# Performance work log

Hardware: AMD Instinct MI355X
Metric: run time of the kernel (lower is better)

Reference implementation:

```python
import jax, jax.numpy as jnp
import numpy as np

B, L, LTXT = 4, 1024, 128
D_MODEL, TEXT_DIM = 768, 768
D_INNER, D_STATE, D_CONV, DT_RANK = 2 * D_MODEL, 16, 4, (D_MODEL + 15) // 16


def setup_inputs() -> dict:
    key = jax.random.key(0)
    ks = jax.random.split(key, 10)
    s = 0.02
    f32 = jnp.float32
    # A_log init as in mamba_ssm: A = repeat(arange(1, d_state+1))
    A_log = jnp.log(jnp.broadcast_to(jnp.arange(1, D_STATE + 1, dtype=f32), (D_INNER, D_STATE)))
    return {
        "image_tokens": jax.random.normal(ks[0], (B, L, D_MODEL), f32),
        "text_tokens": jax.random.normal(ks[1], (B, LTXT, TEXT_DIM), f32),
        "W_txt": s * jax.random.normal(ks[2], (D_MODEL, TEXT_DIM), f32),
        "b_txt": jnp.zeros((D_MODEL,), f32),
        "in_proj_w": s * jax.random.normal(ks[3], (2 * D_INNER, D_MODEL), f32),
        "conv_w": s * jax.random.normal(ks[4], (D_INNER, 1, D_CONV), f32),
        "conv_b": jnp.zeros((D_INNER,), f32),
        "x_proj_w": s * jax.random.normal(ks[5], (DT_RANK + 2 * D_STATE, D_INNER), f32),
        "dt_proj_w": s * jax.random.normal(ks[6], (D_INNER, DT_RANK), f32),
        "dt_proj_b": jnp.full((D_INNER,), -4.6, f32),  # inv-softplus of small dt init
        "A_log": A_log,
        "D": jnp.ones((D_INNER,), f32),
        "out_proj_w": s * jax.random.normal(ks[7], (D_MODEL, D_INNER), f32),
    }


def _mamba(tokens, in_proj_w, conv_w, conv_b, x_proj_w, dt_proj_w, dt_proj_b, A_log, D, out_proj_w):
    Bsz = tokens.shape[0]
    # input projection -> x, z each (B, L, d_inner)
    xz = tokens @ in_proj_w.T
    x, z = jnp.split(xz, 2, axis=-1)
    # causal depthwise conv1d over L + SiLU
    x_bdl = jnp.transpose(x, (0, 2, 1))  # (B, d_inner, L)
    x_conv = jax.lax.conv_general_dilated(
        x_bdl, conv_w, (1,), [(D_CONV - 1, 0)],
        dimension_numbers=("NCH", "OIH", "NCH"), feature_group_count=D_INNER,
    ) + conv_b[None, :, None]
    x = jax.nn.silu(jnp.transpose(x_conv, (0, 2, 1)))  # (B, L, d_inner)
    # input-dependent SSM params
    x_dbl = x @ x_proj_w.T  # (B, L, dt_rank + 2*d_state)
    dt_r = x_dbl[..., :DT_RANK]
    Bm = x_dbl[..., DT_RANK:DT_RANK + D_STATE]  # (B, L, d_state)
    Cm = x_dbl[..., DT_RANK + D_STATE:]         # (B, L, d_state)
    dt = jax.nn.softplus(dt_r @ dt_proj_w.T + dt_proj_b)  # (B, L, d_inner)
    A = -jnp.exp(A_log)  # (d_inner, d_state)

    def step(h, inp):
        dt_t, B_t, C_t, u_t = inp  # (B,d_inner),(B,d_state),(B,d_state),(B,d_inner)
        dA = jnp.exp(dt_t[:, :, None] * A)                  # (B, d_inner, d_state)
        h = dA * h + (dt_t * u_t)[:, :, None] * B_t[:, None, :]
        y = jnp.einsum("bds,bs->bd", h, C_t)
        return h, y

    h0 = jnp.zeros((Bsz, D_INNER, D_STATE), tokens.dtype)
    xs = (
        jnp.transpose(dt, (1, 0, 2)),
        jnp.transpose(Bm, (1, 0, 2)),
        jnp.transpose(Cm, (1, 0, 2)),
        jnp.transpose(x, (1, 0, 2)),
    )
    _, ys = jax.lax.scan(step, h0, xs)  # ys: (L, B, d_inner)
    y = jnp.transpose(ys, (1, 0, 2)) + x * D
    y = y * jax.nn.silu(z)
    return y @ out_proj_w.T  # (B, L, d_model)


def reference(image_tokens, text_tokens, W_txt, b_txt, in_proj_w, conv_w, conv_b,
              x_proj_w, dt_proj_w, dt_proj_b, A_log, D, out_proj_w):
    # text_pool='cls' -> take token 0
    txt = text_tokens[:, 0, :] @ W_txt.T + b_txt          # (B, d_model)
    tokens = image_tokens + txt[:, None, :]                # broadcast add
    y = _mamba(tokens, in_proj_w, conv_w, conv_b, x_proj_w,
               dt_proj_w, dt_proj_b, A_log, D, out_proj_w)
    # AdaptiveAvgPool1d(1) over sequence dim, then squeeze -> (B, d_model)
    return y.mean(axis=1)
```

## Files before the change

### kernel.cpp

```cpp
#include <hip/hip_runtime.h>
#include <math.h>

constexpr int kB   = 4;
constexpr int kL   = 1024;
constexpr int kDM  = 768;
constexpr int kDI  = 1536;
constexpr int kDS  = 16;
constexpr int kDTR = 48;
constexpr int kNX  = 80;
constexpr int kM   = kB * kL;
constexpr int kLTXT = 128;

typedef __attribute__((ext_vector_type(8))) short bf16x8;
typedef __attribute__((ext_vector_type(4))) float f32x4;
typedef __attribute__((ext_vector_type(8))) unsigned short u16x8;

__device__ inline unsigned short f2bf(float f) {
    unsigned u = __float_as_uint(f);
    u = (u + 0x7FFFu + ((u >> 16) & 1u)) >> 16;
    return (unsigned short)u;
}
__device__ inline float bf2f(unsigned short us) {
    return __uint_as_float((unsigned)us << 16);
}

__device__ __forceinline__ void gl2lds16(const unsigned short* g, unsigned short* l) {
    __builtin_amdgcn_global_load_lds(
        (const __attribute__((address_space(1))) unsigned int*)g,
        (__attribute__((address_space(3))) unsigned int*)l, 16, 0, 0);
}

__global__ __launch_bounds__(256) void txt_kernel(
    const float* __restrict__ text, const float* __restrict__ Wt,
    const float* __restrict__ bt, float* __restrict__ txt)
{
    int gw = blockIdx.x * 4 + (threadIdx.x >> 6);
    int lane = threadIdx.x & 63;
    int b = gw / kDM;
    int j = gw - b * kDM;
    const float* trow = text + (size_t)b * kLTXT * kDM;
    const float* wrow = Wt + (size_t)j * kDM;
    float acc = 0.f;
    for (int k = lane; k < kDM; k += 64) acc = fmaf(trow[k], wrow[k], acc);
    #pragma unroll
    for (int o = 32; o; o >>= 1) acc += __shfl_xor(acc, o, 64);
    if (lane == 0) txt[gw] = acc + bt[j];
}

__global__ __launch_bounds__(256) void prep_kernel(
    const float* __restrict__ img, const float* __restrict__ txt,
    unsigned short* __restrict__ tok,
    const float* __restrict__ w, unsigned short* __restrict__ wb)
{
    const int bid = blockIdx.x;
    if (bid < 3072) {
        int i = bid * 256 + threadIdx.x;
        float4 a = ((const float4*)img)[i];
        int m = i / (kDM / 4);
        int k4 = i - m * (kDM / 4);
        float4 tv = ((const float4*)(txt + (size_t)(m >> 10) * kDM))[k4];
        ushort4 o;
        o.x = f2bf(a.x + tv.x); o.y = f2bf(a.y + tv.y);
        o.z = f2bf(a.z + tv.z); o.w = f2bf(a.w + tv.w);
        ((ushort4*)tok)[i] = o;
    } else {
        int i = (bid - 3072) * 256 + threadIdx.x;
        float4 a = ((const float4*)w)[i];
        ushort4 v;
        v.x = f2bf(a.x); v.y = f2bf(a.y); v.z = f2bf(a.z); v.w = f2bf(a.w);
        ((ushort4*)wb)[i] = v;
    }
}

__global__ __launch_bounds__(256) void mfma_inproj_kernel(
    const unsigned short* __restrict__ A, const unsigned short* __restrict__ W,
    float* __restrict__ xout, unsigned short* __restrict__ gout)
{
    __shared__ unsigned short Asm[2][128][32];
    __shared__ unsigned short Wsm[2][128][32];
    const int t = threadIdx.x;
    const int lane = t & 63;
    const int wv = t >> 6;
    const int wr = wv >> 1, wc = wv & 1;
    const int m0 = blockIdx.x * 128;
    const int n0 = blockIdx.y * 128;

    const int srow = lane >> 2;
    const int scol = (lane & 3) * 8;
    const unsigned short* agp  = A + (size_t)(m0 + wv * 32 + srow) * kDM + scol;
    const unsigned short* agp2 = agp + 16 * kDM;
    const unsigned short* wgp  = W + (size_t)(n0 + wv * 32 + srow) * kDM + scol;
    const unsigned short* wgp2 = wgp + 16 * kDM;

    auto stage = [&](int buf, int k0) {
        gl2lds16(agp  + k0, &Asm[buf][wv * 32][0]);
        gl2lds16(agp2 + k0, &Asm[buf][wv * 32 + 16][0]);
        gl2lds16(wgp  + k0, &Wsm[buf][wv * 32][0]);
        gl2lds16(wgp2 + k0, &Wsm[buf][wv * 32 + 16][0]);
    };

    f32x4 acc[4][4] = {};
    const int fr = lane & 15;
    const int fk = (lane >> 4) * 8;

    stage(0, 0);
    __syncthreads();

    int buf = 0;
    for (int k0 = 0; k0 < kDM; k0 += 32) {
        if (k0 + 32 < kDM) stage(buf ^ 1, k0 + 32);
        bf16x8 af[4], wf[4];
        #pragma unroll
        for (int i = 0; i < 4; ++i)
            af[i] = *(const bf16x8*)&Asm[buf][wr * 64 + i * 16 + fr][fk];
        #pragma unroll
        for (int j = 0; j < 4; ++j)
            wf[j] = *(const bf16x8*)&Wsm[buf][wc * 64 + j * 16 + fr][fk];
        #pragma unroll
        for (int i = 0; i < 4; ++i)
            #pragma unroll
            for (int j = 0; j < 4; ++j)
                acc[i][j] = __builtin_amdgcn_mfma_f32_16x16x32_bf16(af[i], wf[j], acc[i][j], 0, 0, 0);
        __syncthreads();
        buf ^= 1;
    }

    const int erow = (lane >> 4) * 4;
    const int ecol = lane & 15;
    #pragma unroll
    for (int i = 0; i < 4; ++i) {
        #pragma unroll
        for (int j = 0; j < 4; ++j) {
            const int gn = n0 + wc * 64 + j * 16 + ecol;
            #pragma unroll
            for (int q = 0; q < 4; ++q) {
                const int gm = m0 + wr * 64 + i * 16 + erow + q;
                float v = acc[i][j][q];
                if (gn < kDI) {
                    xout[(size_t)gm * kDI + gn] = v;
                } else {
                    gout[(size_t)gm * kDI + (gn - kDI)] = f2bf(v / (1.f + __expf(-v)));
                }
            }
        }
    }
}

constexpr int kKS   = 8;
constexpr int kKSEG = kDI / kKS;

__global__ __launch_bounds__(256) void xproj_splitk_kernel(
    const float* __restrict__ A, const float* __restrict__ W,
    float* __restrict__ part)
{
    __shared__ float As[16][68];
    __shared__ float Ws[16][84];
    const int t = threadIdx.x;
    const int m0 = blockIdx.x * 64;
    const int kbase = blockIdx.y * kKSEG;
    const int lrow = t >> 2, lk4 = (t & 3) << 2;
    const int ci = (t & 15) << 2;
    const int cj = (t >> 4) * 5;
    float acc[4][5] = {};
    const float* aptr = A + (size_t)(m0 + lrow) * kDI + kbase + lk4;

    for (int k0 = 0; k0 < kKSEG; k0 += 16) {
        float4 av = *(const float4*)(aptr + k0);
        if (k0) __syncthreads();
        As[lk4+0][lrow] = av.x; As[lk4+1][lrow] = av.y;
        As[lk4+2][lrow] = av.z; As[lk4+3][lrow] = av.w;
        #pragma unroll
        for (int i = 0; i < 5; ++i) {
            int idx = t + 256 * i;
            int n = idx % 80;
            int k = idx / 80;
            Ws[k][n] = W[(size_t)n * kDI + kbase + k0 + k];
        }
        __syncthreads();
        #pragma unroll
        for (int k = 0; k < 16; ++k) {
            const float4 a4 = *(const float4*)&As[k][ci];
            const float aa[4] = {a4.x, a4.y, a4.z, a4.w};
            float ww[5];
            #pragma unroll
            for (int j = 0; j < 5; ++j) ww[j] = Ws[k][cj + j];
            #pragma unroll
            for (int i = 0; i < 4; ++i)
                #pragma unroll
                for (int j = 0; j < 5; ++j)
                    acc[i][j] = fmaf(aa[i], ww[j], acc[i][j]);
        }
    }

    float* pbase = part + ((size_t)blockIdx.y * kM) * kNX;
    #pragma unroll
    for (int i = 0; i < 4; ++i)
        #pragma unroll
        for (int j = 0; j < 5; ++j)
            pbase[(size_t)(m0 + ci + i) * kNX + cj + j] = acc[i][j];
}

__global__ __launch_bounds__(256) void xproj_reduce_kernel(
    const float* __restrict__ part, float* __restrict__ xdbl)
{
    int i = blockIdx.x * 256 + threadIdx.x;
    float s = 0.f;
    #pragma unroll
    for (int k = 0; k < kKS; ++k) s += part[(size_t)k * kM * kNX + i];
    xdbl[i] = s;
}

__global__ __launch_bounds__(256) void dtproj_gemm_kernel(
    const float* __restrict__ A, const float* __restrict__ W,
    const float* __restrict__ bias, unsigned short* __restrict__ dt)
{
    __shared__ float As[16][68];
    __shared__ float Ws[16][68];
    const int t = threadIdx.x;
    const int m0 = blockIdx.x * 64;
    const int n0 = blockIdx.y * 64;
    const int lrow = t >> 2;
    const int lk4  = (t & 3) << 2;
    const int ci   = (t & 15) << 2;
    const int cj   = (t >> 4) << 2;
    float acc[4][4] = {};
    const float* aptr = A + (size_t)(m0 + lrow) * kNX + lk4;
    const float* wptr = W + (size_t)(n0 + lrow) * kDTR + lk4;

    for (int k0 = 0; k0 < kDTR; k0 += 16) {
        float4 av = *(const float4*)(aptr + k0);
        float4 wv = *(const float4*)(wptr + k0);
        if (k0) __syncthreads();
        As[lk4+0][lrow] = av.x; As[lk4+1][lrow] = av.y;
        As[lk4+2][lrow] = av.z; As[lk4+3][lrow] = av.w;
        Ws[lk4+0][lrow] = wv.x; Ws[lk4+1][lrow] = wv.y;
        Ws[lk4+2][lrow] = wv.z; Ws[lk4+3][lrow] = wv.w;
        __syncthreads();
        #pragma unroll
        for (int k = 0; k < 16; ++k) {
            const float4 a4 = *(const float4*)&As[k][ci];
            const float4 w4 = *(const float4*)&Ws[k][cj];
            const float aa[4] = {a4.x, a4.y, a4.z, a4.w};
            const float ww[4] = {w4.x, w4.y, w4.z, w4.w};
            #pragma unroll
            for (int i = 0; i < 4; ++i)
                #pragma unroll
                for (int j = 0; j < 4; ++j)
                    acc[i][j] = fmaf(aa[i], ww[j], acc[i][j]);
        }
    }

    #pragma unroll
    for (int i = 0; i < 4; ++i) {
        const int gm = m0 + ci + i;
        ushort4 o;
        unsigned short* op = (unsigned short*)&o;
        #pragma unroll
        for (int j = 0; j < 4; ++j) {
            float v = acc[i][j] + bias[n0 + cj + j];
            v = (v > 20.f) ? v : log1pf(__expf(v));
            op[j] = f2bf(v);
        }
        *(ushort4*)&dt[(size_t)gm * kDI + n0 + cj] = o;
    }
}

__global__ __launch_bounds__(256) void conv_silu_kernel(
    const float* __restrict__ xraw, const float* __restrict__ cw,
    const float* __restrict__ cb, float* __restrict__ xout)
{
    int i = blockIdx.x * 256 + threadIdx.x;
    int d4 = i % (kDI / 4);
    int ml = i / (kDI / 4);
    int l = ml & (kL - 1);
    const int d = d4 * 4;
    float4 acc = *(const float4*)&cb[d];
    const float* base = xraw + (size_t)ml * kDI + d - 3 * (size_t)kDI;
    float4 w0 = *(const float4*)&cw[(d + 0) * 4];
    float4 w1 = *(const float4*)&cw[(d + 1) * 4];
    float4 w2 = *(const float4*)&cw[(d + 2) * 4];
    float4 w3 = *(const float4*)&cw[(d + 3) * 4];
    const float wj[4][4] = {{w0.x, w1.x, w2.x, w3.x}, {w0.y, w1.y, w2.y, w3.y},
                            {w0.z, w1.z, w2.z, w3.z}, {w0.w, w1.w, w2.w, w3.w}};
    #pragma unroll
    for (int j = 0; j < 4; ++j) {
        if (l - 3 + j >= 0) {
            float4 xv = *(const float4*)(base + (size_t)j * kDI);
            acc.x = fmaf(xv.x, wj[j][0], acc.x);
            acc.y = fmaf(xv.y, wj[j][1], acc.y);
            acc.z = fmaf(xv.z, wj[j][2], acc.z);
            acc.w = fmaf(xv.w, wj[j][3], acc.w);
        }
    }
    acc.x /= (1.f + __expf(-acc.x));
    acc.y /= (1.f + __expf(-acc.y));
    acc.z /= (1.f + __expf(-acc.z));
    acc.w /= (1.f + __expf(-acc.w));
    *(float4*)&xout[(size_t)ml * kDI + d] = acc;
}

constexpr int kNSEG = 16;
constexpr int kSEGL = kL / kNSEG;
constexpr int kCT   = 16;
constexpr int kBD   = kB * kDI;
constexpr int kP    = kBD * 16;
constexpr float kLOG2E = 1.44269504089f;

__global__ __launch_bounds__(256, 6) void scan11_kernel(
    const float* __restrict__ u, const unsigned short* __restrict__ g,
    const unsigned short* __restrict__ dt, const float* __restrict__ xdbl,
    const float* __restrict__ A_log,
    float* __restrict__ PA, float* __restrict__ QA,
    float* __restrict__ accA, float* __restrict__ wcA,
    float* __restrict__ ugA)
{
    __shared__ float uS [kCT][64];
    __shared__ float gS [kCT][64];
    __shared__ float dtS[kCT][64];
    __shared__ float bcS[kCT][34];
    const int t = threadIdx.x;
    const int blk = blockIdx.x;
    const int seg = blk & (kNSEG - 1);
    const int bd  = blk >> 4;
    const int b   = bd / 24;
    const int d0  = (bd % 24) * 64;
    const int c   = t & 63;
    const int sq  = t >> 6;
    const int d   = d0 + c;
    const int lb  = seg * kSEGL;

    f32x4 Av;
    {
        float4 al = *(const float4*)&A_log[d * kDS + sq * 4];
        Av.x = -__expf(al.x) * kLOG2E;
        Av.y = -__expf(al.y) * kLOG2E;
        Av.z = -__expf(al.z) * kLOG2E;
        Av.w = -__expf(al.w) * kLOG2E;
    }

    const float* u_base           = u  + ((size_t)b << 10) * kDI + d0;
    const unsigned short* g_base  = g  + ((size_t)b << 10) * kDI + d0;
    const unsigned short* dt_base = dt + ((size_t)b << 10) * kDI + d0;
    const float* bc_base = xdbl + ((size_t)b << 10) * kNX + kDTR;
    const int sr = t >> 4, scn = (t & 15) * 4;
    const int hr = (t & 127) >> 3, hc = ((t & 127) & 7) * 8;
    const int rb = (t & 127) >> 3, cbo = ((t & 127) & 7) * 4;

    float4 ru, rbc;
    u16x8 rgd;
    auto load_chunk = [&](int l0) {
        ru = *(const float4*)(u_base + (size_t)(l0 + sr) * kDI + scn);
        if (t < 128) {
            rgd = *(const u16x8*)(g_base + (size_t)(l0 + hr) * kDI + hc);
            rbc = *(const float4*)(bc_base + (size_t)(l0 + rb) * kNX + cbo);
        } else {
            rgd = *(const u16x8*)(dt_base + (size_t)(l0 + hr) * kDI + hc);
        }
    };
    auto store_chunk = [&]() {
        *(float4*)&uS[sr][scn] = ru;
        float* dst = (t < 128) ? &gS[hr][hc] : &dtS[hr][hc];
        float4 lo, hi;
        lo.x = bf2f(rgd[0]); lo.y = bf2f(rgd[1]);
        lo.z = bf2f(rgd[2]); lo.w = bf2f(rgd[3]);
        hi.x = bf2f(rgd[4]); hi.y = bf2f(rgd[5]);
        hi.z = bf2f(rgd[6]); hi.w = bf2f(rgd[7]);
        *(float4*)(dst)     = lo;
        *(float4*)(dst + 4) = hi;
        if (t < 128) *(float4*)&bcS[rb][cbo] = rbc;
    };

    f32x4 h   = {0.f, 0.f, 0.f, 0.f};
    f32x4 cp  = {1.f, 1.f, 1.f, 1.f};
    f32x4 acc = {0.f, 0.f, 0.f, 0.f};
    f32x4 wc  = {0.f, 0.f, 0.f, 0.f};
    float ug = 0.f;

    load_chunk(lb);
    store_chunk();
    __syncthreads();

    #pragma unroll
    for (int ck = 0; ck < kSEGL / kCT; ++ck) {
        if (ck + 1 < kSEGL / kCT) load_chunk(lb + (ck + 1) * kCT);
        #pragma unroll 8
        for (int i = 0; i < kCT; ++i) {
            const float dtv = dtS[i][c];
            const float uv  = uS [i][c];
            const float gv  = gS [i][c];
            const f32x4 Bv = *(const f32x4*)&bcS[i][sq * 4];
            const f32x4 Cv = *(const f32x4*)&bcS[i][16 + sq * 4];
            const f32x4 pm = dtv * Av;
            f32x4 dA;
            dA.x = exp2f(pm.x); dA.y = exp2f(pm.y);
            dA.z = exp2f(pm.z); dA.w = exp2f(pm.w);
            const float dtu = dtv * uv;
            h  = dA * h + dtu * Bv;
            cp = cp * dA;
            const f32x4 cg = Cv * gv;
            acc = h * cg + acc;
            wc  = cp * cg + wc;
            ug  = fmaf(uv, gv, ug);
        }
        if (ck + 1 < kSEGL / kCT) {
            __syncthreads();
            store_chunk();
            __syncthreads();
        }
    }

    const size_t o = (size_t)seg * kP + ((size_t)sq * kBD + b * kDI + d) * 4;
    *(f32x4*)&PA[o]   = cp;
    *(f32x4*)&QA[o]   = h;
    *(f32x4*)&accA[o] = acc;
    *(f32x4*)&wcA[o]  = wc;
    if (sq == 0) ugA[(size_t)seg * kBD + b * kDI + d] = ug;
}

__global__ __launch_bounds__(256) void scan_combine_kernel(
    const float* __restrict__ PA, const float* __restrict__ QA,
    const float* __restrict__ accA, const float* __restrict__ wcA,
    const float* __restrict__ ugA, const float* __restrict__ Dvec,
    float* __restrict__ ysum)
{
    const int p = blockIdx.x * 256 + threadIdx.x;
    const int s = p & 15;
    const int bd = p >> 4;
    const size_t pbase = ((size_t)(s >> 2) * kBD + bd) * 4 + (s & 3);
    float h = 0.f, tot = 0.f;
    #pragma unroll
    for (int seg = 0; seg < kNSEG; ++seg) {
        const size_t o = (size_t)seg * kP + pbase;
        tot += accA[o] + h * wcA[o];
        h = fmaf(PA[o], h, QA[o]);
    }
    #pragma unroll
    for (int o2 = 1; o2 < 16; o2 <<= 1) tot += __shfl_xor(tot, o2, 64);
    if (s == 0) {
        float ug = 0.f;
        #pragma unroll
        for (int seg = 0; seg < kNSEG; ++seg)
            ug += ugA[(size_t)seg * kBD + bd];
        ysum[bd] = tot + Dvec[bd % kDI] * ug;
    }
}

__global__ __launch_bounds__(256) void final_kernel(
    const float* __restrict__ ysum, const float* __restrict__ Wout,
    float* __restrict__ out)
{
    int gw = blockIdx.x * 4 + (threadIdx.x >> 6);
    int lane = threadIdx.x & 63;
    int b = gw / kDM;
    int j = gw - b * kDM;
    const float* yrow = ysum + (size_t)b * kDI;
    const float* wrow = Wout + (size_t)j * kDI;
    float acc = 0.f;
    for (int k = lane; k < kDI; k += 64) acc = fmaf(yrow[k], wrow[k], acc);
    #pragma unroll
    for (int o = 32; o; o >>= 1) acc += __shfl_xor(acc, o, 64);
    if (lane == 0) out[gw] = acc * (1.f / (float)kL);
}

extern "C" void kernel_launch(void* const* d_in, const int* in_sizes, int n_in,
                              void* d_out, int out_size, void* d_ws, size_t ws_size,
                              hipStream_t stream)
{
    const float* image_tokens = (const float*)d_in[0];
    const float* text_tokens  = (const float*)d_in[1];
    const float* W_txt        = (const float*)d_in[2];
    const float* b_txt        = (const float*)d_in[3];
    const float* in_proj_w    = (const float*)d_in[4];
    const float* conv_w       = (const float*)d_in[5];
    const float* conv_b       = (const float*)d_in[6];
    const float* x_proj_w     = (const float*)d_in[7];
    const float* dt_proj_w    = (const float*)d_in[8];
    const float* dt_proj_b    = (const float*)d_in[9];
    const float* A_log        = (const float*)d_in[10];
    const float* Dvec         = (const float*)d_in[11];
    const float* out_proj_w   = (const float*)d_in[12];
    float* out = (float*)d_out;

    char* p = (char*)d_ws;
    float* txt  = (float*)p;                      p += 12288;
    float* dtreg = (float*)p;                     p += (size_t)kM * kDI * 4;
    float* xraw = (float*)p;                      p += (size_t)kM * kDI * 4;
    unsigned short* gbuf = (unsigned short*)p;    p += (size_t)kM * kDI * 4;
    float* xbuf = (float*)p;                      p += (size_t)kM * kDI * 4;
    float* xdbl = (float*)p;                      p += (size_t)kM * kNX * 4;
    float* ysum = (float*)p;                      p += 32768;
    float* ugA  = (float*)p;                      p += (size_t)kNSEG * kBD * 4;

    unsigned short* tokb = (unsigned short*)dtreg;
    unsigned short* wb   = tokb + (size_t)kM * kDM;
    float* part = dtreg;
    unsigned short* dtb = (unsigned short*)dtreg;
    float* PA   = xraw;
    float* QA   = PA + (size_t)kNSEG * kP;
    float* accA = QA + (size_t)kNSEG * kP;
    float* wcA  = accA + (size_t)kNSEG * kP;

    txt_kernel<<<dim3(kB * kDM / 4), dim3(256), 0, stream>>>(text_tokens, W_txt, b_txt, txt);

    prep_kernel<<<dim3(3072 + 2304), dim3(256), 0, stream>>>(
        image_tokens, txt, tokb, in_proj_w, wb);

    mfma_inproj_kernel<<<dim3(kM / 128, 2 * kDI / 128), dim3(256), 0, stream>>>(
        tokb, wb, xraw, gbuf);

    conv_silu_kernel<<<dim3(kM * kDI / 4 / 256), dim3(256), 0, stream>>>(
        xraw, conv_w, conv_b, xbuf);

    xproj_splitk_kernel<<<dim3(kM / 64, kKS), dim3(256), 0, stream>>>(xbuf, x_proj_w, part);
    xproj_reduce_kernel<<<dim3(kM * kNX / 256), dim3(256), 0, stream>>>(part, xdbl);

    dtproj_gemm_kernel<<<dim3(kM / 64, kDI / 64), dim3(256), 0, stream>>>(
        xdbl, dt_proj_w, dt_proj_b, dtb);

    scan11_kernel<<<dim3(kB * 24 * kNSEG), dim3(256), 0, stream>>>(
        xbuf, gbuf, dtb, xdbl, A_log, PA, QA, accA, wcA, ugA);
    scan_combine_kernel<<<dim3(kP / 256), dim3(256), 0, stream>>>(
        PA, QA, accA, wcA, ugA, Dvec, ysum);

    final_kernel<<<dim3(kB * kDM / 4), dim3(256), 0, stream>>>(ysum, out_proj_w, out);
}
```

Baseline: 185.5 us.

## Store x pre-conv and post-conv activations in bf16 across kernels

```diff
diff --git a/kernel.cpp b/kernel.cpp
--- a/kernel.cpp
+++ b/kernel.cpp
@@ -74,7 +74,7 @@
 
 __global__ __launch_bounds__(256) void mfma_inproj_kernel(
     const unsigned short* __restrict__ A, const unsigned short* __restrict__ W,
-    float* __restrict__ xout, unsigned short* __restrict__ gout)
+    unsigned short* __restrict__ xout, unsigned short* __restrict__ gout)
 {
     __shared__ unsigned short Asm[2][128][32];
     __shared__ unsigned short Wsm[2][128][32];
@@ -137,7 +137,7 @@
                 const int gm = m0 + wr * 64 + i * 16 + erow + q;
                 float v = acc[i][j][q];
                 if (gn < kDI) {
-                    xout[(size_t)gm * kDI + gn] = v;
+                    xout[(size_t)gm * kDI + gn] = f2bf(v);
                 } else {
                     gout[(size_t)gm * kDI + (gn - kDI)] = f2bf(v / (1.f + __expf(-v)));
                 }
@@ -146,11 +146,43 @@
     }
 }
 
+__global__ __launch_bounds__(256) void conv_silu_kernel(
+    const unsigned short* __restrict__ xraw, const float* __restrict__ cw,
+    const float* __restrict__ cb, unsigned short* __restrict__ xout)
+{
+    int i = blockIdx.x * 256 + threadIdx.x;
+    int d8 = i % (kDI / 8);
+    int ml = i / (kDI / 8);
+    int l = ml & (kL - 1);
+    const int d = d8 * 8;
+    float acc[8];
+    *(float4*)&acc[0] = *(const float4*)&cb[d];
+    *(float4*)&acc[4] = *(const float4*)&cb[d + 4];
+    const unsigned short* base = xraw + (size_t)ml * kDI + d - 3 * (size_t)kDI;
+    float4 cwv[8];
+    #pragma unroll
+    for (int e = 0; e < 8; ++e) cwv[e] = *(const float4*)&cw[(d + e) * 4];
+    #pragma unroll
+    for (int j = 0; j < 4; ++j) {
+        if (l - 3 + j >= 0) {
+            u16x8 xv = *(const u16x8*)(base + (size_t)j * kDI);
+            #pragma unroll
+            for (int e = 0; e < 8; ++e)
+                acc[e] = fmaf(bf2f(xv[e]), ((const float*)&cwv[e])[j], acc[e]);
+        }
+    }
+    u16x8 o;
+    #pragma unroll
+    for (int e = 0; e < 8; ++e)
+        o[e] = f2bf(acc[e] / (1.f + __expf(-acc[e])));
+    *(u16x8*)(xout + (size_t)ml * kDI + d) = o;
+}
+
 constexpr int kKS   = 8;
 constexpr int kKSEG = kDI / kKS;
 
 __global__ __launch_bounds__(256) void xproj_splitk_kernel(
-    const float* __restrict__ A, const float* __restrict__ W,
+    const unsigned short* __restrict__ A, const float* __restrict__ W,
     float* __restrict__ part)
 {
     __shared__ float As[16][68];
@@ -162,13 +194,13 @@
     const int ci = (t & 15) << 2;
     const int cj = (t >> 4) * 5;
     float acc[4][5] = {};
-    const float* aptr = A + (size_t)(m0 + lrow) * kDI + kbase + lk4;
+    const unsigned short* aptr = A + (size_t)(m0 + lrow) * kDI + kbase + lk4;
 
     for (int k0 = 0; k0 < kKSEG; k0 += 16) {
-        float4 av = *(const float4*)(aptr + k0);
+        ushort4 av = *(const ushort4*)(aptr + k0);
         if (k0) __syncthreads();
-        As[lk4+0][lrow] = av.x; As[lk4+1][lrow] = av.y;
-        As[lk4+2][lrow] = av.z; As[lk4+3][lrow] = av.w;
+        As[lk4+0][lrow] = bf2f(av.x); As[lk4+1][lrow] = bf2f(av.y);
+        As[lk4+2][lrow] = bf2f(av.z); As[lk4+3][lrow] = bf2f(av.w);
         #pragma unroll
         for (int i = 0; i < 5; ++i) {
             int idx = t + 256 * i;
@@ -265,40 +297,6 @@
     }
 }
 
-__global__ __launch_bounds__(256) void conv_silu_kernel(
-    const float* __restrict__ xraw, const float* __restrict__ cw,
-    const float* __restrict__ cb, float* __restrict__ xout)
-{
-    int i = blockIdx.x * 256 + threadIdx.x;
-    int d4 = i % (kDI / 4);
-    int ml = i / (kDI / 4);
-    int l = ml & (kL - 1);
-    const int d = d4 * 4;
-    float4 acc = *(const float4*)&cb[d];
-    const float* base = xraw + (size_t)ml * kDI + d - 3 * (size_t)kDI;
-    float4 w0 = *(const float4*)&cw[(d + 0) * 4];
-    float4 w1 = *(const float4*)&cw[(d + 1) * 4];
-    float4 w2 = *(const float4*)&cw[(d + 2) * 4];
-    float4 w3 = *(const float4*)&cw[(d + 3) * 4];
-    const float wj[4][4] = {{w0.x, w1.x, w2.x, w3.x}, {w0.y, w1.y, w2.y, w3.y},
-                            {w0.z, w1.z, w2.z, w3.z}, {w0.w, w1.w, w2.w, w3.w}};
-    #pragma unroll
-    for (int j = 0; j < 4; ++j) {
-        if (l - 3 + j >= 0) {
-            float4 xv = *(const float4*)(base + (size_t)j * kDI);
-            acc.x = fmaf(xv.x, wj[j][0], acc.x);
-            acc.y = fmaf(xv.y, wj[j][1], acc.y);
-            acc.z = fmaf(xv.z, wj[j][2], acc.z);
-            acc.w = fmaf(xv.w, wj[j][3], acc.w);
-        }
-    }
-    acc.x /= (1.f + __expf(-acc.x));
-    acc.y /= (1.f + __expf(-acc.y));
-    acc.z /= (1.f + __expf(-acc.z));
-    acc.w /= (1.f + __expf(-acc.w));
-    *(float4*)&xout[(size_t)ml * kDI + d] = acc;
-}
-
 constexpr int kNSEG = 16;
 constexpr int kSEGL = kL / kNSEG;
 constexpr int kCT   = 16;
@@ -306,8 +304,8 @@
 constexpr int kP    = kBD * 16;
 constexpr float kLOG2E = 1.44269504089f;
 
-__global__ __launch_bounds__(256, 6) void scan11_kernel(
-    const float* __restrict__ u, const unsigned short* __restrict__ g,
+__global__ __launch_bounds__(256, 6) void scan12_kernel(
+    const unsigned short* __restrict__ u, const unsigned short* __restrict__ g,
     const unsigned short* __restrict__ dt, const float* __restrict__ xdbl,
     const float* __restrict__ A_log,
     float* __restrict__ PA, float* __restrict__ QA,
@@ -338,36 +336,46 @@
         Av.w = -__expf(al.w) * kLOG2E;
     }
 
-    const float* u_base           = u  + ((size_t)b << 10) * kDI + d0;
+    const unsigned short* u_base  = u  + ((size_t)b << 10) * kDI + d0;
     const unsigned short* g_base  = g  + ((size_t)b << 10) * kDI + d0;
     const unsigned short* dt_base = dt + ((size_t)b << 10) * kDI + d0;
     const float* bc_base = xdbl + ((size_t)b << 10) * kNX + kDTR;
-    const int sr = t >> 4, scn = (t & 15) * 4;
-    const int hr = (t & 127) >> 3, hc = ((t & 127) & 7) * 8;
-    const int rb = (t & 127) >> 3, cbo = ((t & 127) & 7) * 4;
-
-    float4 ru, rbc;
-    u16x8 rgd;
+    const int th = t & 127;
+    const int hr = th >> 3, hc = (th & 7) * 8;
+    const int rb = th >> 3, cbo = (th & 7) * 4;
+
+    u16x8 r0, r1;
+    float4 rbc;
     auto load_chunk = [&](int l0) {
-        ru = *(const float4*)(u_base + (size_t)(l0 + sr) * kDI + scn);
         if (t < 128) {
-            rgd = *(const u16x8*)(g_base + (size_t)(l0 + hr) * kDI + hc);
+            r0  = *(const u16x8*)(u_base + (size_t)(l0 + hr) * kDI + hc);
             rbc = *(const float4*)(bc_base + (size_t)(l0 + rb) * kNX + cbo);
         } else {
-            rgd = *(const u16x8*)(dt_base + (size_t)(l0 + hr) * kDI + hc);
+            r0 = *(const u16x8*)(g_base  + (size_t)(l0 + hr) * kDI + hc);
+            r1 = *(const u16x8*)(dt_base + (size_t)(l0 + hr) * kDI + hc);
         }
     };
     auto store_chunk = [&]() {
-        *(float4*)&uS[sr][scn] = ru;
-        float* dst = (t < 128) ? &gS[hr][hc] : &dtS[hr][hc];
         float4 lo, hi;
-        lo.x = bf2f(rgd[0]); lo.y = bf2f(rgd[1]);
-        lo.z = bf2f(rgd[2]); lo.w = bf2f(rgd[3]);
-        hi.x = bf2f(rgd[4]); hi.y = bf2f(rgd[5]);
-        hi.z = bf2f(rgd[6]); hi.w = bf2f(rgd[7]);
-        *(float4*)(dst)     = lo;
-        *(float4*)(dst + 4) = hi;
-        if (t < 128) *(float4*)&bcS[rb][cbo] = rbc;
+        lo.x = bf2f(r0[0]); lo.y = bf2f(r0[1]);
+        lo.z = bf2f(r0[2]); lo.w = bf2f(r0[3]);
+        hi.x = bf2f(r0[4]); hi.y = bf2f(r0[5]);
+        hi.z = bf2f(r0[6]); hi.w = bf2f(r0[7]);
+        if (t < 128) {
+            *(float4*)&uS[hr][hc]     = lo;
+            *(float4*)&uS[hr][hc + 4] = hi;
+            *(float4*)&bcS[rb][cbo]   = rbc;
+        } else {
+            *(float4*)&gS[hr][hc]     = lo;
+            *(float4*)&gS[hr][hc + 4] = hi;
+            float4 l2, h2;
+            l2.x = bf2f(r1[0]); l2.y = bf2f(r1[1]);
+            l2.z = bf2f(r1[2]); l2.w = bf2f(r1[3]);
+            h2.x = bf2f(r1[4]); h2.y = bf2f(r1[5]);
+            h2.z = bf2f(r1[6]); h2.w = bf2f(r1[7]);
+            *(float4*)&dtS[hr][hc]     = l2;
+            *(float4*)&dtS[hr][hc + 4] = h2;
+        }
     };
 
     f32x4 h   = {0.f, 0.f, 0.f, 0.f};
@@ -484,9 +492,9 @@
     char* p = (char*)d_ws;
     float* txt  = (float*)p;                      p += 12288;
     float* dtreg = (float*)p;                     p += (size_t)kM * kDI * 4;
-    float* xraw = (float*)p;                      p += (size_t)kM * kDI * 4;
-    unsigned short* gbuf = (unsigned short*)p;    p += (size_t)kM * kDI * 4;
-    float* xbuf = (float*)p;                      p += (size_t)kM * kDI * 4;
+    float* xrawR = (float*)p;                     p += (size_t)kM * kDI * 4;
+    unsigned short* gbuf = (unsigned short*)p;    p += (size_t)kM * kDI * 2;
+    unsigned short* xbuf = (unsigned short*)p;    p += (size_t)kM * kDI * 2;
     float* xdbl = (float*)p;                      p += (size_t)kM * kNX * 4;
     float* ysum = (float*)p;                      p += 32768;
     float* ugA  = (float*)p;                      p += (size_t)kNSEG * kBD * 4;
@@ -495,7 +503,8 @@
     unsigned short* wb   = tokb + (size_t)kM * kDM;
     float* part = dtreg;
     unsigned short* dtb = (unsigned short*)dtreg;
-    float* PA   = xraw;
+    unsigned short* xraw = (unsigned short*)xrawR;
+    float* PA   = xrawR;
     float* QA   = PA + (size_t)kNSEG * kP;
     float* accA = QA + (size_t)kNSEG * kP;
     float* wcA  = accA + (size_t)kNSEG * kP;
@@ -508,7 +517,7 @@
     mfma_inproj_kernel<<<dim3(kM / 128, 2 * kDI / 128), dim3(256), 0, stream>>>(
         tokb, wb, xraw, gbuf);
 
-    conv_silu_kernel<<<dim3(kM * kDI / 4 / 256), dim3(256), 0, stream>>>(
+    conv_silu_kernel<<<dim3(kM * kDI / 8 / 256), dim3(256), 0, stream>>>(
         xraw, conv_w, conv_b, xbuf);
 
     xproj_splitk_kernel<<<dim3(kM / 64, kKS), dim3(256), 0, stream>>>(xbuf, x_proj_w, part);
@@ -517,7 +526,7 @@
     dtproj_gemm_kernel<<<dim3(kM / 64, kDI / 64), dim3(256), 0, stream>>>(
         xdbl, dt_proj_w, dt_proj_b, dtb);
 
-    scan11_kernel<<<dim3(kB * 24 * kNSEG), dim3(256), 0, stream>>>(
+    scan12_kernel<<<dim3(kB * 24 * kNSEG), dim3(256), 0, stream>>>(
         xbuf, gbuf, dtb, xdbl, A_log, PA, QA, accA, wcA, ugA);
     scan_combine_kernel<<<dim3(kP / 256), dim3(256), 0, stream>>>(
         PA, QA, accA, wcA, ugA, Dvec, ysum);
```

After: 188.9 us. No clear change (+1.9%).
